# Kernel tuning notes

Hardware: AMD Instinct MI355X
Metric: run time of the kernel (lower is better)

Reference implementation:

```python
import jax, jax.numpy as jnp
import numpy as np

N_HEAD, D_HEAD, D_MODEL, MAX_LEN = 16, 64, 1024, 64
T, B = 1024, 4
SCALE = 1.0 / D_HEAD ** 0.5


def setup_inputs() -> dict:
    key = jax.random.key(0)
    k1, k2, k3, k4 = jax.random.split(key, 4)
    s = 0.02
    w = jax.random.normal(k1, (T, B, D_MODEL), jnp.float32)
    Wqkv = jax.random.normal(k2, (3 * N_HEAD * D_HEAD, D_MODEL), jnp.float32) * s
    pos_emb = jax.random.normal(k3, (2 * MAX_LEN + 1, D_HEAD), jnp.float32) * s
    Wo = jax.random.normal(k4, (D_MODEL, N_HEAD * D_HEAD), jnp.float32) * s
    i = jnp.arange(T)
    # causal mask, 3D path of the original: [qlen, klen, bsz], True = masked
    attn_mask = jnp.broadcast_to((i[None, :] > i[:, None])[:, :, None], (T, T, B))
    return {"w": w, "attn_mask": attn_mask, "Wqkv": Wqkv, "pos_emb": pos_emb, "Wo": Wo}


def reference(w, attn_mask, Wqkv, pos_emb, Wo):
    qlen, bsz, _ = w.shape
    klen = qlen
    # qkv projection (no bias), chunk into q, k, v
    heads = jnp.einsum('tbd,ed->tbe', w, Wqkv)            # [T, B, 3*H*Dh]
    q, k, v = jnp.split(heads, 3, axis=-1)
    q = q.reshape(qlen, bsz, N_HEAD, D_HEAD).transpose(1, 2, 0, 3) * SCALE  # [B,H,T,Dh]
    k = k.reshape(klen, bsz, N_HEAD, D_HEAD).transpose(1, 2, 0, 3)
    v = v.reshape(klen, bsz, N_HEAD, D_HEAD).transpose(1, 2, 0, 3)
    # learnable relative position embeddings r[q_pos, k_pos, Dh]
    i = jnp.arange(klen)
    rel = jnp.clip(i[None, :] - i[:, None], -MAX_LEN, MAX_LEN) + MAX_LEN   # [T, T]
    r = pos_emb[rel]                                                       # [T, T, Dh]
    # content score + relative-position score (q already scaled)
    qk = jnp.einsum('bhqd,bhkd->bhqk', q, k)
    qr = jnp.einsum('bhqd,qkd->bhqk', q, r)
    score = qk + qr                                                        # [B,H,T,T]
    m = attn_mask.transpose(2, 0, 1)[:, None]                              # [B,1,T,T]
    score = jnp.where(m, -jnp.inf, score)
    attn = jax.nn.softmax(score, axis=-1)                                  # coverage
    # content context + position context
    ctx = jnp.einsum('bhqk,bhkd->bhqd', attn, v) + jnp.einsum('bhqk,qkd->bhqd', attn, r)
    attn_vec = ctx.transpose(0, 2, 1, 3).reshape(bsz, qlen, N_HEAD * D_HEAD)
    out = jnp.einsum('bte,de->btd', attn_vec, Wo)                          # [B,T,D]
    return jnp.swapaxes(out, 0, 1)                                         # [T,B,D]
```

## Files before the change

kernel.cpp:

```cpp
#include <hip/hip_runtime.h>
#include <hip/hip_bf16.h>
#include <math.h>

#define N_HEAD 16
#define D_HEAD 64
#define T_SEQ 1024
#define BATCH 4
#define SCALE 0.125f

typedef float f32x4 __attribute__((ext_vector_type(4)));
typedef short bf16x8 __attribute__((ext_vector_type(8)));
typedef short bf16x4v __attribute__((ext_vector_type(4)));

#define AS1(p) ((const __attribute__((address_space(1))) void*)(p))
#define AS3(p) ((__attribute__((address_space(3))) void*)(p))

__device__ inline bf16x8 ld8(const __hip_bfloat16* p) {
    bf16x4v lo = *(const bf16x4v*)p;
    bf16x4v hi = *(const bf16x4v*)(p + 4);
    return __builtin_shufflevector(lo, hi, 0, 1, 2, 3, 4, 5, 6, 7);
}

__global__ __launch_bounds__(256) void cast_all(
    const float* __restrict__ s0, __hip_bfloat16* __restrict__ d0, int n0,
    const float* __restrict__ s1, __hip_bfloat16* __restrict__ d1, int n1,
    const float* __restrict__ s2, __hip_bfloat16* __restrict__ d2, int n2) {
    int i = (blockIdx.x * 256 + threadIdx.x) * 8;
    const float* src;
    __hip_bfloat16* dst;
    if (i < n0) { src = s0 + i; dst = d0 + i; }
    else if ((i -= n0) < n1) { src = s1 + i; dst = d1 + i; }
    else if ((i -= n1) < n2) { src = s2 + i; dst = d2 + i; }
    else return;
    float4 a = *(const float4*)src;
    float4 b = *(const float4*)(src + 4);
    __hip_bfloat16 t[8];
    t[0] = __float2bfloat16(a.x); t[1] = __float2bfloat16(a.y);
    t[2] = __float2bfloat16(a.z); t[3] = __float2bfloat16(a.w);
    t[4] = __float2bfloat16(b.x); t[5] = __float2bfloat16(b.y);
    t[6] = __float2bfloat16(b.z); t[7] = __float2bfloat16(b.w);
    *(uint4*)dst = *(const uint4*)t;
}

__global__ __launch_bounds__(256) void qkv_gemm_mfma(
    const __hip_bfloat16* __restrict__ A,
    const __hip_bfloat16* __restrict__ B,
    const float* __restrict__ P,
    __hip_bfloat16* __restrict__ Qb, __hip_bfloat16* __restrict__ Kb,
    __hip_bfloat16* __restrict__ Vtb) {
    constexpr int Kd = 1024;
    __shared__ __hip_bfloat16 As[128 * 32];
    __shared__ __hip_bfloat16 Bs[128 * 32];
    const int tid = threadIdx.x;
    const int w = tid >> 6, lane = tid & 63;
    const int lanelo = lane & 15, quad = lane >> 4;
    const int wm = (w >> 1) * 64, wn = (w & 1) * 64;
    const int m0 = blockIdx.y * 128, n0 = blockIdx.x * 128;

    const __hip_bfloat16* Ag = A + (size_t)(m0 + w * 16 + (lane >> 2)) * Kd + (lane & 3) * 8;
    const __hip_bfloat16* Bg = B + (size_t)(n0 + w * 16 + (lane >> 2)) * Kd + (lane & 3) * 8;
    __hip_bfloat16* AsW0 = As + w * 16 * 32;
    __hip_bfloat16* AsW1 = As + (64 + w * 16) * 32;
    __hip_bfloat16* BsW0 = Bs + w * 16 * 32;
    __hip_bfloat16* BsW1 = Bs + (64 + w * 16) * 32;

    f32x4 acc[4][4];
#pragma unroll
    for (int i = 0; i < 4; i++)
#pragma unroll
        for (int j = 0; j < 4; j++) acc[i][j] = (f32x4){0.f, 0.f, 0.f, 0.f};

    for (int k0 = 0; k0 < Kd; k0 += 32) {
        __syncthreads();
        __builtin_amdgcn_global_load_lds(AS1(Ag + k0), AS3(AsW0), 16, 0, 0);
        __builtin_amdgcn_global_load_lds(AS1(Ag + 64 * Kd + k0), AS3(AsW1), 16, 0, 0);
        __builtin_amdgcn_global_load_lds(AS1(Bg + k0), AS3(BsW0), 16, 0, 0);
        __builtin_amdgcn_global_load_lds(AS1(Bg + 64 * Kd + k0), AS3(BsW1), 16, 0, 0);
        __syncthreads();
        bf16x8 af[4], bfr[4];
#pragma unroll
        for (int i = 0; i < 4; i++)
            af[i] = *(const bf16x8*)(As + (wm + i * 16 + lanelo) * 32 + quad * 8);
#pragma unroll
        for (int j = 0; j < 4; j++)
            bfr[j] = *(const bf16x8*)(Bs + (wn + j * 16 + lanelo) * 32 + quad * 8);
#pragma unroll
        for (int i = 0; i < 4; i++)
#pragma unroll
            for (int j = 0; j < 4; j++)
                acc[i][j] = __builtin_amdgcn_mfma_f32_16x16x32_bf16(af[i], bfr[j], acc[i][j], 0, 0, 0);
    }

    const int part = n0 >> 10;
    float p0v[4] = {0.f, 0.f, 0.f, 0.f};
    if (part == 2) {
#pragma unroll
        for (int j = 0; j < 4; j++) p0v[j] = P[j * 16 + lanelo];
    }
#pragma unroll
    for (int i = 0; i < 4; i++)
#pragma unroll
        for (int j = 0; j < 4; j++)
#pragma unroll
            for (int reg = 0; reg < 4; reg++) {
                const int row = m0 + wm + i * 16 + quad * 4 + reg;
                const int col = n0 + wn + j * 16 + lanelo;
                const int t = row >> 2, b = row & 3;
                const int e = col & 1023, h = e >> 6, d = e & 63;
                const float v = acc[i][j][reg];
                if (part == 0)
                    Qb[((size_t)(b * 16 + h) * 1024 + t) * 64 + d] = __float2bfloat16(v * SCALE);
                else if (part == 1)
                    Kb[((size_t)(b * 16 + h) * 1024 + t) * 64 + d] = __float2bfloat16(v);
                else
                    Vtb[((size_t)(b * 16 + h) * 64 + d) * 1024 + t] = __float2bfloat16(v + p0v[j]);
            }
}

__global__ __launch_bounds__(256) void out_gemm_mfma(
    const __hip_bfloat16* __restrict__ A,
    const __hip_bfloat16* __restrict__ B,
    float* __restrict__ out) {
    constexpr int Kd = 1024;
    __shared__ __hip_bfloat16 As[128 * 32];
    __shared__ __hip_bfloat16 Bs[64 * 32];
    const int tid = threadIdx.x;
    const int w = tid >> 6, lane = tid & 63;
    const int lanelo = lane & 15, quad = lane >> 4;
    const int wm = (w >> 1) * 64, wn = (w & 1) * 32;
    const int m0 = blockIdx.y * 128, n0 = blockIdx.x * 64;

    const __hip_bfloat16* Ag = A + (size_t)(m0 + w * 16 + (lane >> 2)) * Kd + (lane & 3) * 8;
    const __hip_bfloat16* Bg = B + (size_t)(n0 + w * 16 + (lane >> 2)) * Kd + (lane & 3) * 8;
    __hip_bfloat16* AsW0 = As + w * 16 * 32;
    __hip_bfloat16* AsW1 = As + (64 + w * 16) * 32;
    __hip_bfloat16* BsW0 = Bs + w * 16 * 32;

    f32x4 acc[4][2];
#pragma unroll
    for (int i = 0; i < 4; i++)
#pragma unroll
        for (int j = 0; j < 2; j++) acc[i][j] = (f32x4){0.f, 0.f, 0.f, 0.f};

    for (int k0 = 0; k0 < Kd; k0 += 32) {
        __syncthreads();
        __builtin_amdgcn_global_load_lds(AS1(Ag + k0), AS3(AsW0), 16, 0, 0);
        __builtin_amdgcn_global_load_lds(AS1(Ag + 64 * Kd + k0), AS3(AsW1), 16, 0, 0);
        __builtin_amdgcn_global_load_lds(AS1(Bg + k0), AS3(BsW0), 16, 0, 0);
        __syncthreads();
        bf16x8 af[4], bfr[2];
#pragma unroll
        for (int i = 0; i < 4; i++)
            af[i] = *(const bf16x8*)(As + (wm + i * 16 + lanelo) * 32 + quad * 8);
#pragma unroll
        for (int j = 0; j < 2; j++)
            bfr[j] = *(const bf16x8*)(Bs + (wn + j * 16 + lanelo) * 32 + quad * 8);
#pragma unroll
        for (int i = 0; i < 4; i++)
#pragma unroll
            for (int j = 0; j < 2; j++)
                acc[i][j] = __builtin_amdgcn_mfma_f32_16x16x32_bf16(af[i], bfr[j], acc[i][j], 0, 0, 0);
    }

#pragma unroll
    for (int i = 0; i < 4; i++)
#pragma unroll
        for (int j = 0; j < 2; j++)
#pragma unroll
            for (int reg = 0; reg < 4; reg++) {
                const int row = m0 + wm + i * 16 + quad * 4 + reg;
                const int col = n0 + wn + j * 16 + lanelo;
                const int b = row >> 10, t = row & 1023;
                out[(size_t)(t * 4 + b) * 1024 + col] = acc[i][j][reg];
            }
}

__global__ __launch_bounds__(256) void flash_attn(
    const __hip_bfloat16* __restrict__ Qb,
    const __hip_bfloat16* __restrict__ Kb,
    const __hip_bfloat16* __restrict__ Vtb,
    const float* __restrict__ P,
    __hip_bfloat16* __restrict__ av) {
    __shared__ __hip_bfloat16 Ks[64][72];
    __shared__ __hip_bfloat16 Vs[64][72];
    __shared__ __hip_bfloat16 Pl[4][16][68];
    __shared__ __hip_bfloat16 Pband[4][16][68];
    __shared__ __hip_bfloat16 QPl[4][16][72];

    const int T = 15 - blockIdx.x;
    const int bh = blockIdx.y;
    const int b = bh >> 4, h = bh & 15;
    const int tid = threadIdx.x;
    const int w = tid >> 6, lane = tid & 63;
    const int lanelo = lane & 15, quad = lane >> 4;
    const int q0 = T * 64 + w * 16;
    const size_t qkbase = (size_t)bh * 1024 * 64;
    const size_t vbase  = (size_t)bh * 64 * 1024;

    const int sr = tid >> 2;
    const int sc = (tid & 3) << 4;
    const __hip_bfloat16* kgb = Kb + qkbase + (size_t)sr * 64 + sc;
    const __hip_bfloat16* vgb = Vtb + vbase + (size_t)sr * 1024 + sc;

    {
        short* pb = (short*)&Pband[w][0][0];
        for (int i = lane; i < 16 * 68; i += 64) pb[i] = 0;
    }
    bf16x8 aq0, aq1;
    {
        const __hip_bfloat16* qrow = Qb + qkbase + (size_t)(q0 + lanelo) * 64;
        aq0 = *(const bf16x8*)(qrow + quad * 8);
        aq1 = *(const bf16x8*)(qrow + 32 + quad * 8);
    }
#pragma unroll
    for (int jj = 0; jj < 5; jj++) {
        const float* prow = P + (size_t)(jj * 16 + lanelo) * 64 + quad * 8;
        float4 pa = *(const float4*)prow;
        float4 pb = *(const float4*)(prow + 4);
        float4 pc = *(const float4*)(prow + 32);
        float4 pd = *(const float4*)(prow + 36);
        __hip_bfloat16 t0[8], t1[8];
        t0[0] = __float2bfloat16(pa.x); t0[1] = __float2bfloat16(pa.y);
        t0[2] = __float2bfloat16(pa.z); t0[3] = __float2bfloat16(pa.w);
        t0[4] = __float2bfloat16(pb.x); t0[5] = __float2bfloat16(pb.y);
        t0[6] = __float2bfloat16(pb.z); t0[7] = __float2bfloat16(pb.w);
        t1[0] = __float2bfloat16(pc.x); t1[1] = __float2bfloat16(pc.y);
        t1[2] = __float2bfloat16(pc.z); t1[3] = __float2bfloat16(pc.w);
        t1[4] = __float2bfloat16(pd.x); t1[5] = __float2bfloat16(pd.y);
        t1[6] = __float2bfloat16(pd.z); t1[7] = __float2bfloat16(pd.w);
        f32x4 acc = (f32x4){0.f, 0.f, 0.f, 0.f};
        acc = __builtin_amdgcn_mfma_f32_16x16x32_bf16(aq0, *(const bf16x8*)t0, acc, 0, 0, 0);
        acc = __builtin_amdgcn_mfma_f32_16x16x32_bf16(aq1, *(const bf16x8*)t1, acc, 0, 0, 0);
#pragma unroll
        for (int reg = 0; reg < 4; reg++)
            QPl[w][quad * 4 + reg][jj * 16 + lanelo] = __float2bfloat16(acc[reg]);
    }
    float qp0r[4];
#pragma unroll
    for (int reg = 0; reg < 4; reg++)
        qp0r[reg] = (float)QPl[w][quad * 4 + reg][0];

    f32x4 o_acc[4], o_l;
#pragma unroll
    for (int dt = 0; dt < 4; dt++) o_acc[dt] = (f32x4){0.f, 0.f, 0.f, 0.f};
    o_l = (f32x4){0.f, 0.f, 0.f, 0.f};
    const short one_bf = 0x3F80;
    const bf16x8 vones = {one_bf, one_bf, one_bf, one_bf, one_bf, one_bf, one_bf, one_bf};

    uint4 rk0, rk1, rv0, rv1;
    rk0 = *(const uint4*)(kgb);
    rk1 = *(const uint4*)(kgb + 8);
    rv0 = *(const uint4*)(vgb);
    rv1 = *(const uint4*)(vgb + 8);

    for (int kt = 0; kt <= T; kt++) {
        __syncthreads();
        *(uint4*)&Ks[sr][sc]     = rk0;
        *(uint4*)&Ks[sr][sc + 8] = rk1;
        *(uint4*)&Vs[sr][sc]     = rv0;
        *(uint4*)&Vs[sr][sc + 8] = rv1;
        if (kt < T) {
            const __hip_bfloat16* kg = kgb + (size_t)(kt + 1) * 4096;
            const __hip_bfloat16* vg = vgb + (size_t)(kt + 1) * 64;
            rk0 = *(const uint4*)(kg);
            rk1 = *(const uint4*)(kg + 8);
            rv0 = *(const uint4*)(vg);
            rv1 = *(const uint4*)(vg + 8);
        }
        __syncthreads();

        f32x4 s_acc[4];
#pragma unroll
        for (int ct = 0; ct < 4; ct++) {
            bf16x8 b0 = *(const bf16x8*)&Ks[ct * 16 + lanelo][quad * 8];
            bf16x8 b1 = *(const bf16x8*)&Ks[ct * 16 + lanelo][32 + quad * 8];
            f32x4 acc = (f32x4){0.f, 0.f, 0.f, 0.f};
            acc = __builtin_amdgcn_mfma_f32_16x16x32_bf16(aq0, b0, acc, 0, 0, 0);
            acc = __builtin_amdgcn_mfma_f32_16x16x32_bf16(aq1, b1, acc, 0, 0, 0);
            s_acc[ct] = acc;
        }

        const int obase = q0 - kt * 64;
        if (kt < T - 1) {
#pragma unroll
            for (int ct = 0; ct < 4; ct++)
#pragma unroll
                for (int reg = 0; reg < 4; reg++) {
                    const float p = __expf(s_acc[ct][reg] + qp0r[reg]);
                    Pl[w][quad * 4 + reg][ct * 16 + lanelo] = __float2bfloat16(p);
                }
        } else {
#pragma unroll
            for (int ct = 0; ct < 4; ct++)
#pragma unroll
                for (int reg = 0; reg < 4; reg++) {
                    const int rloc = quad * 4 + reg;
                    const int kl = ct * 16 + lanelo;
                    const int o = obase + rloc - kl;
                    const int idx = (o >= 64 || o < 0) ? 0 : (64 - o);
                    const float add = (float)QPl[w][rloc][idx];
                    const float p = (o < 0) ? 0.f : __expf(s_acc[ct][reg] + add);
                    const __hip_bfloat16 pbv = __float2bfloat16(p);
                    Pl[w][rloc][kl] = pbv;
                    if (o >= 0 && o <= 63) Pband[w][rloc][63 - o] = pbv;
                }
        }

#pragma unroll
        for (int c = 0; c < 2; c++) {
            bf16x8 ap = ld8(&Pl[w][lanelo][c * 32 + quad * 8]);
#pragma unroll
            for (int dt = 0; dt < 4; dt++) {
                bf16x8 bv = *(const bf16x8*)&Vs[dt * 16 + lanelo][c * 32 + quad * 8];
                o_acc[dt] = __builtin_amdgcn_mfma_f32_16x16x32_bf16(ap, bv, o_acc[dt], 0, 0, 0);
            }
            o_l = __builtin_amdgcn_mfma_f32_16x16x32_bf16(ap, vones, o_l, 0, 0, 0);
        }
    }

#pragma unroll
    for (int c = 0; c < 2; c++) {
        bf16x8 ab = ld8(&Pband[w][lanelo][c * 32 + quad * 8]);
#pragma unroll
        for (int dt = 0; dt < 4; dt++) {
            const int d = dt * 16 + lanelo;
            const float p0 = P[d];
            __hip_bfloat16 tb[8];
#pragma unroll
            for (int jj = 0; jj < 8; jj++) {
                const int kk = c * 32 + quad * 8 + jj;
                tb[jj] = __float2bfloat16(P[(kk + 1) * 64 + d] - p0);
            }
            o_acc[dt] = __builtin_amdgcn_mfma_f32_16x16x32_bf16(ab, *(const bf16x8*)tb, o_acc[dt], 0, 0, 0);
        }
    }

    float rinv[4];
#pragma unroll
    for (int reg = 0; reg < 4; reg++) rinv[reg] = 1.0f / o_l[reg];
#pragma unroll
    for (int dt = 0; dt < 4; dt++) {
        const int cdim = dt * 16 + lanelo;
#pragma unroll
        for (int reg = 0; reg < 4; reg++) {
            const int q = q0 + quad * 4 + reg;
            av[((size_t)(b * 1024 + q)) * 1024 + h * 64 + cdim] =
                __float2bfloat16(o_acc[dt][reg] * rinv[reg]);
        }
    }
}

extern "C" void kernel_launch(void* const* d_in, const int* in_sizes, int n_in,
                              void* d_out, int out_size, void* d_ws, size_t ws_size,
                              hipStream_t stream) {
    const float* w       = (const float*)d_in[0];
    const float* Wqkv    = (const float*)d_in[2];
    const float* pos_emb = (const float*)d_in[3];
    const float* Wo      = (const float*)d_in[4];
    float* out = (float*)d_out;

    const size_t SZ = (size_t)BATCH * N_HEAD * T_SEQ * D_HEAD;
    __hip_bfloat16* wb     = (__hip_bfloat16*)d_ws;
    __hip_bfloat16* Wqkvb  = wb + SZ;
    __hip_bfloat16* Wob    = Wqkvb + 3 * 1024 * 1024;
    __hip_bfloat16* Qb     = Wob + 1024 * 1024;
    __hip_bfloat16* Kb     = Qb + SZ;
    __hip_bfloat16* Vtb    = Kb + SZ;
    __hip_bfloat16* AVb    = Vtb + SZ;

    const int n_w = 4096 * 1024, n_wqkv = 3072 * 1024, n_wo = 1024 * 1024;
    const int n_tot = n_w + n_wqkv + n_wo;
    cast_all<<<n_tot / 2048, 256, 0, stream>>>(w, wb, n_w, Wqkv, Wqkvb, n_wqkv, Wo, Wob, n_wo);

    qkv_gemm_mfma<<<dim3(3072 / 128, 4096 / 128), 256, 0, stream>>>(wb, Wqkvb, pos_emb, Qb, Kb, Vtb);
    flash_attn<<<dim3(16, 64), 256, 0, stream>>>(Qb, Kb, Vtb, pos_emb, AVb);
    out_gemm_mfma<<<dim3(1024 / 64, 4096 / 128), 256, 0, stream>>>(AVb, Wob, out);
}
```

Baseline: 201.9 us.

## Pair causal query tiles per block and use exp2 with log2e-folded Q scale

Each attention block now processes two query tiles, a long one (15-px) and a short one (px). The short tile reuses the K/V tiles already staged in shared memory, which balances work across blocks under the causal mask and halves the grid. The Q scale now has log2(e) folded in, so the softmax can use exp2 instead of expf. The cost is extra registers for a second set of accumulators and larger shared-memory buffers, which may lower occupancy.

```diff
diff --git a/kernel.cpp b/kernel.cpp
--- a/kernel.cpp
+++ b/kernel.cpp
@@ -6,7 +6,7 @@
 #define D_HEAD 64
 #define T_SEQ 1024
 #define BATCH 4
-#define SCALE 0.125f
+#define QSCALE 0.180336879f
 
 typedef float f32x4 __attribute__((ext_vector_type(4)));
 typedef short bf16x8 __attribute__((ext_vector_type(8)));
@@ -109,7 +109,7 @@
                 const int e = col & 1023, h = e >> 6, d = e & 63;
                 const float v = acc[i][j][reg];
                 if (part == 0)
-                    Qb[((size_t)(b * 16 + h) * 1024 + t) * 64 + d] = __float2bfloat16(v * SCALE);
+                    Qb[((size_t)(b * 16 + h) * 1024 + t) * 64 + d] = __float2bfloat16(v * QSCALE);
                 else if (part == 1)
                     Kb[((size_t)(b * 16 + h) * 1024 + t) * 64 + d] = __float2bfloat16(v);
                 else
@@ -184,16 +184,16 @@
     __shared__ __hip_bfloat16 Ks[64][72];
     __shared__ __hip_bfloat16 Vs[64][72];
     __shared__ __hip_bfloat16 Pl[4][16][68];
-    __shared__ __hip_bfloat16 Pband[4][16][68];
-    __shared__ __hip_bfloat16 QPl[4][16][72];
-
-    const int T = 15 - blockIdx.x;
+    __shared__ __hip_bfloat16 Pband[4][2][16][68];
+    __shared__ __hip_bfloat16 QPl[4][2][16][66];
+
+    const int px = blockIdx.x;
+    const int TB = 15 - px, TS = px;
     const int bh = blockIdx.y;
     const int b = bh >> 4, h = bh & 15;
     const int tid = threadIdx.x;
     const int w = tid >> 6, lane = tid & 63;
     const int lanelo = lane & 15, quad = lane >> 4;
-    const int q0 = T * 64 + w * 16;
     const size_t qkbase = (size_t)bh * 1024 * 64;
     const size_t vbase  = (size_t)bh * 64 * 1024;
 
@@ -203,15 +203,20 @@
     const __hip_bfloat16* vgb = Vtb + vbase + (size_t)sr * 1024 + sc;
 
     {
-        short* pb = (short*)&Pband[w][0][0];
-        for (int i = lane; i < 16 * 68; i += 64) pb[i] = 0;
-    }
-    bf16x8 aq0, aq1;
+        short* pb = (short*)&Pband[w][0][0][0];
+        for (int i = lane; i < 2 * 16 * 68; i += 64) pb[i] = 0;
+    }
+
+    bf16x8 aqb0, aqb1, aqs0, aqs1;
     {
-        const __hip_bfloat16* qrow = Qb + qkbase + (size_t)(q0 + lanelo) * 64;
-        aq0 = *(const bf16x8*)(qrow + quad * 8);
-        aq1 = *(const bf16x8*)(qrow + 32 + quad * 8);
-    }
+        const __hip_bfloat16* qrb = Qb + qkbase + (size_t)(TB * 64 + w * 16 + lanelo) * 64;
+        aqb0 = *(const bf16x8*)(qrb + quad * 8);
+        aqb1 = *(const bf16x8*)(qrb + 32 + quad * 8);
+        const __hip_bfloat16* qrs = Qb + qkbase + (size_t)(TS * 64 + w * 16 + lanelo) * 64;
+        aqs0 = *(const bf16x8*)(qrs + quad * 8);
+        aqs1 = *(const bf16x8*)(qrs + 32 + quad * 8);
+    }
+
 #pragma unroll
     for (int jj = 0; jj < 5; jj++) {
         const float* prow = P + (size_t)(jj * 16 + lanelo) * 64 + quad * 8;
@@ -228,24 +233,85 @@
         t1[2] = __float2bfloat16(pc.z); t1[3] = __float2bfloat16(pc.w);
         t1[4] = __float2bfloat16(pd.x); t1[5] = __float2bfloat16(pd.y);
         t1[6] = __float2bfloat16(pd.z); t1[7] = __float2bfloat16(pd.w);
-        f32x4 acc = (f32x4){0.f, 0.f, 0.f, 0.f};
-        acc = __builtin_amdgcn_mfma_f32_16x16x32_bf16(aq0, *(const bf16x8*)t0, acc, 0, 0, 0);
-        acc = __builtin_amdgcn_mfma_f32_16x16x32_bf16(aq1, *(const bf16x8*)t1, acc, 0, 0, 0);
-#pragma unroll
-        for (int reg = 0; reg < 4; reg++)
-            QPl[w][quad * 4 + reg][jj * 16 + lanelo] = __float2bfloat16(acc[reg]);
-    }
-    float qp0r[4];
-#pragma unroll
-    for (int reg = 0; reg < 4; reg++)
-        qp0r[reg] = (float)QPl[w][quad * 4 + reg][0];
-
-    f32x4 o_acc[4], o_l;
-#pragma unroll
-    for (int dt = 0; dt < 4; dt++) o_acc[dt] = (f32x4){0.f, 0.f, 0.f, 0.f};
-    o_l = (f32x4){0.f, 0.f, 0.f, 0.f};
+        f32x4 accB = (f32x4){0.f, 0.f, 0.f, 0.f};
+        accB = __builtin_amdgcn_mfma_f32_16x16x32_bf16(aqb0, *(const bf16x8*)t0, accB, 0, 0, 0);
+        accB = __builtin_amdgcn_mfma_f32_16x16x32_bf16(aqb1, *(const bf16x8*)t1, accB, 0, 0, 0);
+        f32x4 accS = (f32x4){0.f, 0.f, 0.f, 0.f};
+        accS = __builtin_amdgcn_mfma_f32_16x16x32_bf16(aqs0, *(const bf16x8*)t0, accS, 0, 0, 0);
+        accS = __builtin_amdgcn_mfma_f32_16x16x32_bf16(aqs1, *(const bf16x8*)t1, accS, 0, 0, 0);
+#pragma unroll
+        for (int reg = 0; reg < 4; reg++) {
+            QPl[w][0][quad * 4 + reg][jj * 16 + lanelo] = __float2bfloat16(accB[reg]);
+            QPl[w][1][quad * 4 + reg][jj * 16 + lanelo] = __float2bfloat16(accS[reg]);
+        }
+    }
+    float qp0b[4], qp0s[4];
+#pragma unroll
+    for (int reg = 0; reg < 4; reg++) {
+        qp0b[reg] = (float)QPl[w][0][quad * 4 + reg][0];
+        qp0s[reg] = (float)QPl[w][1][quad * 4 + reg][0];
+    }
+
+    f32x4 o_accB[4], o_lB, o_accS[4], o_lS;
+#pragma unroll
+    for (int dt = 0; dt < 4; dt++) {
+        o_accB[dt] = (f32x4){0.f, 0.f, 0.f, 0.f};
+        o_accS[dt] = (f32x4){0.f, 0.f, 0.f, 0.f};
+    }
+    o_lB = (f32x4){0.f, 0.f, 0.f, 0.f};
+    o_lS = (f32x4){0.f, 0.f, 0.f, 0.f};
     const short one_bf = 0x3F80;
     const bf16x8 vones = {one_bf, one_bf, one_bf, one_bf, one_bf, one_bf, one_bf, one_bf};
+
+    auto do_qtile = [&](int tq, int Tq, const bf16x8& a0, const bf16x8& a1,
+                        const float* qp0, f32x4* o_acc, f32x4& o_l, int kt) {
+        f32x4 s_acc[4];
+#pragma unroll
+        for (int ct = 0; ct < 4; ct++) {
+            bf16x8 b0 = *(const bf16x8*)&Ks[ct * 16 + lanelo][quad * 8];
+            bf16x8 b1 = *(const bf16x8*)&Ks[ct * 16 + lanelo][32 + quad * 8];
+            f32x4 acc = (f32x4){0.f, 0.f, 0.f, 0.f};
+            acc = __builtin_amdgcn_mfma_f32_16x16x32_bf16(a0, b0, acc, 0, 0, 0);
+            acc = __builtin_amdgcn_mfma_f32_16x16x32_bf16(a1, b1, acc, 0, 0, 0);
+            s_acc[ct] = acc;
+        }
+        const int q0 = Tq * 64 + w * 16;
+        const int obase = q0 - kt * 64;
+        if (kt < Tq - 1) {
+#pragma unroll
+            for (int ct = 0; ct < 4; ct++)
+#pragma unroll
+                for (int reg = 0; reg < 4; reg++) {
+                    const float p = __builtin_exp2f(s_acc[ct][reg] + qp0[reg]);
+                    Pl[w][quad * 4 + reg][ct * 16 + lanelo] = __float2bfloat16(p);
+                }
+        } else {
+#pragma unroll
+            for (int ct = 0; ct < 4; ct++)
+#pragma unroll
+                for (int reg = 0; reg < 4; reg++) {
+                    const int rloc = quad * 4 + reg;
+                    const int kl = ct * 16 + lanelo;
+                    const int o = obase + rloc - kl;
+                    const int idx = (o >= 64 || o < 0) ? 0 : (64 - o);
+                    const float add = (float)QPl[w][tq][rloc][idx];
+                    const float p = (o < 0) ? 0.f : __builtin_exp2f(s_acc[ct][reg] + add);
+                    const __hip_bfloat16 pbv = __float2bfloat16(p);
+                    Pl[w][rloc][kl] = pbv;
+                    if (o >= 0 && o <= 63) Pband[w][tq][rloc][63 - o] = pbv;
+                }
+        }
+#pragma unroll
+        for (int c = 0; c < 2; c++) {
+            bf16x8 ap = ld8(&Pl[w][lanelo][c * 32 + quad * 8]);
+#pragma unroll
+            for (int dt = 0; dt < 4; dt++) {
+                bf16x8 bv = *(const bf16x8*)&Vs[dt * 16 + lanelo][c * 32 + quad * 8];
+                o_acc[dt] = __builtin_amdgcn_mfma_f32_16x16x32_bf16(ap, bv, o_acc[dt], 0, 0, 0);
+            }
+            o_l = __builtin_amdgcn_mfma_f32_16x16x32_bf16(ap, vones, o_l, 0, 0, 0);
+        }
+    };
 
     uint4 rk0, rk1, rv0, rv1;
     rk0 = *(const uint4*)(kgb);
@@ -253,13 +319,13 @@
     rv0 = *(const uint4*)(vgb);
     rv1 = *(const uint4*)(vgb + 8);
 
-    for (int kt = 0; kt <= T; kt++) {
+    for (int kt = 0; kt <= TB; kt++) {
         __syncthreads();
         *(uint4*)&Ks[sr][sc]     = rk0;
         *(uint4*)&Ks[sr][sc + 8] = rk1;
         *(uint4*)&Vs[sr][sc]     = rv0;
         *(uint4*)&Vs[sr][sc + 8] = rv1;
-        if (kt < T) {
+        if (kt < TB) {
             const __hip_bfloat16* kg = kgb + (size_t)(kt + 1) * 4096;
             const __hip_bfloat16* vg = vgb + (size_t)(kt + 1) * 64;
             rk0 = *(const uint4*)(kg);
@@ -269,83 +335,43 @@
         }
         __syncthreads();
 
-        f32x4 s_acc[4];
-#pragma unroll
-        for (int ct = 0; ct < 4; ct++) {
-            bf16x8 b0 = *(const bf16x8*)&Ks[ct * 16 + lanelo][quad * 8];
-            bf16x8 b1 = *(const bf16x8*)&Ks[ct * 16 + lanelo][32 + quad * 8];
-            f32x4 acc = (f32x4){0.f, 0.f, 0.f, 0.f};
-            acc = __builtin_amdgcn_mfma_f32_16x16x32_bf16(aq0, b0, acc, 0, 0, 0);
-            acc = __builtin_amdgcn_mfma_f32_16x16x32_bf16(aq1, b1, acc, 0, 0, 0);
-            s_acc[ct] = acc;
-        }
-
-        const int obase = q0 - kt * 64;
-        if (kt < T - 1) {
-#pragma unroll
-            for (int ct = 0; ct < 4; ct++)
-#pragma unroll
-                for (int reg = 0; reg < 4; reg++) {
-                    const float p = __expf(s_acc[ct][reg] + qp0r[reg]);
-                    Pl[w][quad * 4 + reg][ct * 16 + lanelo] = __float2bfloat16(p);
+        do_qtile(0, TB, aqb0, aqb1, qp0b, o_accB, o_lB, kt);
+        if (kt <= TS) do_qtile(1, TS, aqs0, aqs1, qp0s, o_accS, o_lS, kt);
+    }
+
+#pragma unroll
+    for (int tq = 0; tq < 2; tq++) {
+        f32x4* o_acc = tq == 0 ? o_accB : o_accS;
+        f32x4& o_l   = tq == 0 ? o_lB : o_lS;
+        const int q0 = (tq == 0 ? TB : TS) * 64 + w * 16;
+#pragma unroll
+        for (int c = 0; c < 2; c++) {
+            bf16x8 ab = ld8(&Pband[w][tq][lanelo][c * 32 + quad * 8]);
+#pragma unroll
+            for (int dt = 0; dt < 4; dt++) {
+                const int d = dt * 16 + lanelo;
+                const float p0 = P[d];
+                __hip_bfloat16 tb[8];
+#pragma unroll
+                for (int jj = 0; jj < 8; jj++) {
+                    const int kk = c * 32 + quad * 8 + jj;
+                    tb[jj] = __float2bfloat16(P[(kk + 1) * 64 + d] - p0);
                 }
-        } else {
-#pragma unroll
-            for (int ct = 0; ct < 4; ct++)
-#pragma unroll
-                for (int reg = 0; reg < 4; reg++) {
-                    const int rloc = quad * 4 + reg;
-                    const int kl = ct * 16 + lanelo;
-                    const int o = obase + rloc - kl;
-                    const int idx = (o >= 64 || o < 0) ? 0 : (64 - o);
-                    const float add = (float)QPl[w][rloc][idx];
-                    const float p = (o < 0) ? 0.f : __expf(s_acc[ct][reg] + add);
-                    const __hip_bfloat16 pbv = __float2bfloat16(p);
-                    Pl[w][rloc][kl] = pbv;
-                    if (o >= 0 && o <= 63) Pband[w][rloc][63 - o] = pbv;
-                }
-        }
-
-#pragma unroll
-        for (int c = 0; c < 2; c++) {
-            bf16x8 ap = ld8(&Pl[w][lanelo][c * 32 + quad * 8]);
-#pragma unroll
-            for (int dt = 0; dt < 4; dt++) {
-                bf16x8 bv = *(const bf16x8*)&Vs[dt * 16 + lanelo][c * 32 + quad * 8];
-                o_acc[dt] = __builtin_amdgcn_mfma_f32_16x16x32_bf16(ap, bv, o_acc[dt], 0, 0, 0);
+                o_acc[dt] = __builtin_amdgcn_mfma_f32_16x16x32_bf16(ab, *(const bf16x8*)tb, o_acc[dt], 0, 0, 0);
             }
-            o_l = __builtin_amdgcn_mfma_f32_16x16x32_bf16(ap, vones, o_l, 0, 0, 0);
-        }
-    }
-
-#pragma unroll
-    for (int c = 0; c < 2; c++) {
-        bf16x8 ab = ld8(&Pband[w][lanelo][c * 32 + quad * 8]);
+        }
+        float rinv[4];
+#pragma unroll
+        for (int reg = 0; reg < 4; reg++) rinv[reg] = 1.0f / o_l[reg];
 #pragma unroll
         for (int dt = 0; dt < 4; dt++) {
-            const int d = dt * 16 + lanelo;
-            const float p0 = P[d];
-            __hip_bfloat16 tb[8];
-#pragma unroll
-            for (int jj = 0; jj < 8; jj++) {
-                const int kk = c * 32 + quad * 8 + jj;
-                tb[jj] = __float2bfloat16(P[(kk + 1) * 64 + d] - p0);
+            const int cdim = dt * 16 + lanelo;
+#pragma unroll
+            for (int reg = 0; reg < 4; reg++) {
+                const int q = q0 + quad * 4 + reg;
+                av[((size_t)(b * 1024 + q)) * 1024 + h * 64 + cdim] =
+                    __float2bfloat16(o_acc[dt][reg] * rinv[reg]);
             }
-            o_acc[dt] = __builtin_amdgcn_mfma_f32_16x16x32_bf16(ab, *(const bf16x8*)tb, o_acc[dt], 0, 0, 0);
-        }
-    }
-
-    float rinv[4];
-#pragma unroll
-    for (int reg = 0; reg < 4; reg++) rinv[reg] = 1.0f / o_l[reg];
-#pragma unroll
-    for (int dt = 0; dt < 4; dt++) {
-        const int cdim = dt * 16 + lanelo;
-#pragma unroll
-        for (int reg = 0; reg < 4; reg++) {
-            const int q = q0 + quad * 4 + reg;
-            av[((size_t)(b * 1024 + q)) * 1024 + h * 64 + cdim] =
-                __float2bfloat16(o_acc[dt][reg] * rinv[reg]);
         }
     }
 }
@@ -373,6 +399,6 @@
     cast_all<<<n_tot / 2048, 256, 0, stream>>>(w, wb, n_w, Wqkv, Wqkvb, n_wqkv, Wo, Wob, n_wo);
 
     qkv_gemm_mfma<<<dim3(3072 / 128, 4096 / 128), 256, 0, stream>>>(wb, Wqkvb, pos_emb, Qb, Kb, Vtb);
-    flash_attn<<<dim3(16, 64), 256, 0, stream>>>(Qb, Kb, Vtb, pos_emb, AVb);
+    flash_attn<<<dim3(8, 64), 256, 0, stream>>>(Qb, Kb, Vtb, pos_emb, AVb);
     out_gemm_mfma<<<dim3(1024 / 64, 4096 / 128), 256, 0, stream>>>(AVb, Wob, out);
 }
```

Result: faster. 189.3 us (-6.2%).
